# Optimization experiments

Measured on AMD Instinct MI355X. Metric: run time of the kernel, lower is better.

The kernel has to match this reference:

```python
import math
import jax, jax.numpy as jnp
import numpy as np

B, S, D, H, DK = 2, 2048, 1024, 16, 64
NUM_BUCKETS, MAX_DISTANCE = 32, 128


def _relative_position_bucket(rel_pos):
    # bidirectional=True (encoder): is_decoder=False
    nb = NUM_BUCKETS // 2
    rel_buckets = (rel_pos > 0).astype(jnp.int32) * nb
    rp = jnp.abs(rel_pos)
    max_exact = nb // 2
    is_small = rp < max_exact
    rp_large = max_exact + (
        jnp.log(rp.astype(jnp.float32) / max_exact)
        / math.log(MAX_DISTANCE / max_exact)
        * (nb - max_exact)
    ).astype(jnp.int32)
    rp_large = jnp.minimum(rp_large, nb - 1)
    return rel_buckets + jnp.where(is_small, rp, rp_large)


def compute_bias(rel_bias, q_len, k_len):
    ctx = jnp.arange(q_len, dtype=jnp.int32)[:, None]
    mem = jnp.arange(k_len, dtype=jnp.int32)[None, :]
    buckets = _relative_position_bucket(mem - ctx)          # [q,k]
    vals = rel_bias[buckets]                                 # [q,k,H]
    return jnp.transpose(vals, (2, 0, 1))[None]              # [1,H,q,k]


def setup_inputs() -> dict:
    key = jax.random.key(0)
    ks = jax.random.split(key, 6)
    scale = 0.02
    return {
        "hidden_states": jax.random.normal(ks[0], (B, S, D), jnp.float32),
        "Wq": jax.random.normal(ks[1], (D, H * DK), jnp.float32) * scale,
        "Wk": jax.random.normal(ks[2], (D, H * DK), jnp.float32) * scale,
        "Wv": jax.random.normal(ks[3], (D, H * DK), jnp.float32) * scale,
        "Wo": jax.random.normal(ks[4], (H * DK, D), jnp.float32) * scale,
        "rel_bias": jax.random.normal(ks[5], (NUM_BUCKETS, H), jnp.float32) * scale,
    }


def reference(hidden_states, Wq, Wk, Wv, Wo, rel_bias):
    b, s, _ = hidden_states.shape

    def shape(x):  # [b,s,H*DK] -> [b,H,s,DK]
        return x.reshape(b, s, H, DK).transpose(0, 2, 1, 3)

    q = shape(hidden_states @ Wq)
    k = shape(hidden_states @ Wk)
    v = shape(hidden_states @ Wv)

    # T5: no 1/sqrt(d_k) scaling
    scores = jnp.einsum("bhqd,bhkd->bhqk", q, k)
    position_bias = compute_bias(rel_bias, s, s)             # [1,H,s,s]
    scores = scores + position_bias
    attn = jax.nn.softmax(scores.astype(jnp.float32), axis=-1).astype(scores.dtype)
    out = jnp.einsum("bhqk,bhkd->bhqd", attn, v)
    out = out.transpose(0, 2, 1, 3).reshape(b, s, H * DK)
    return out @ Wo
```

## Files before the change

kernel.cpp:

```cpp
#include <hip/hip_runtime.h>

#define HH 16
#define DKK 64
#define SS 2048
#define BB 2
#define DD 1024

typedef __attribute__((ext_vector_type(4))) float f32x4;
typedef __attribute__((ext_vector_type(16))) float f32x16;
typedef __attribute__((ext_vector_type(8))) short bf16x8;
typedef __attribute__((ext_vector_type(4))) short s16x4;
typedef __attribute__((ext_vector_type(4))) int i32x4;

#define WAITCNT_VM0 0xF70

__device__ __forceinline__ short bf16b(float f) {
    union { float f; unsigned u; } x; x.f = f;
    unsigned r = (x.u + 0x7fffu + ((x.u >> 16) & 1u)) >> 16;
    return (short)r;
}

__device__ __forceinline__ f32x4 mfma16(bf16x8 a, bf16x8 b, f32x4 c) {
    return __builtin_amdgcn_mfma_f32_16x16x32_bf16(a, b, c, 0, 0, 0);
}

__device__ __forceinline__ f32x16 mfma32(bf16x8 a, bf16x8 b, f32x16 c) {
    return __builtin_amdgcn_mfma_f32_32x32x16_bf16(a, b, c, 0, 0, 0);
}

__device__ __forceinline__ void lds16(const short* g, short* l) {
    __builtin_amdgcn_global_load_lds(
        (const __attribute__((address_space(1))) void*)g,
        (__attribute__((address_space(3))) void*)l, 16, 0, 0);
}

__device__ __forceinline__ int cvtpk(float lo, float hi) {
    int r;
    asm("v_cvt_pk_bf16_f32 %0, %1, %2" : "=v"(r) : "v"(lo), "v"(hi));
    return r;
}

__device__ __forceinline__ void swap32(int& a, int& b) {
    asm("v_permlane32_swap_b32 %0, %1" : "+v"(a), "+v"(b));
}

__global__ __launch_bounds__(256) void prep(
    const float* __restrict__ hs,
    const float* __restrict__ W0, const float* __restrict__ W1,
    const float* __restrict__ W2, const float* __restrict__ W3,
    const float* __restrict__ rb,
    short* __restrict__ hsb,
    short* __restrict__ T0, short* __restrict__ T1,
    short* __restrict__ T2, short* __restrict__ T3,
    float* __restrict__ tab) {
    __shared__ short tile[32][33];
    int blk = blockIdx.x, tid = threadIdx.x;
    if (blk < 4096) {
        int i = (blk * 256 + tid) * 4;
        f32x4 v = *(const f32x4*)(hs + i);
        s16x4 o;
        o.x = bf16b(v.x); o.y = bf16b(v.y); o.z = bf16b(v.z); o.w = bf16b(v.w);
        *(s16x4*)(hsb + i) = o;
    } else if (blk < 8192) {
        int t = blk - 4096;
        int z = t >> 10, r = t & 1023;
        int bx = r & 31, by = r >> 5;
        const float* W; short* T;
        switch (z) {
            case 0: W = W0; T = T0; break;
            case 1: W = W1; T = T1; break;
            case 2: W = W2; T = T2; break;
            default: W = W3; T = T3; break;
        }
        int n0 = bx * 32, k0 = by * 32;
        int tx = tid & 31, ty = (tid >> 5) * 4;
#pragma unroll
        for (int i = 0; i < 4; i++)
            tile[ty + i][tx] = bf16b(W[(k0 + ty + i) * DD + n0 + tx]);
        __syncthreads();
#pragma unroll
        for (int i = 0; i < 4; i++)
            T[(n0 + ty + i) * DD + k0 + tx] = tile[tx][ty + i];
    } else {
        int idx = (blk - 8192) * 256 + tid;
        if (idx < HH * 4095) {
            int h = idx / 4095, d = idx % 4095;
            int rel = d - 2047;
            int bucket = (rel > 0) ? 16 : 0;
            unsigned rr = (rel < 0) ? (unsigned)(-rel) : (unsigned)rel;
            int add;
            if (rr < 8) add = (int)rr;
            else {
                int e = 31 - __clz(rr);
                unsigned long long r2 = (unsigned long long)rr * (unsigned long long)rr;
                int f = 2 * e + ((r2 >= (2ull << (2 * e))) ? 1 : 0);
                add = 8 + (f - 6);
                if (add > 15) add = 15;
            }
            bucket += add;
            tab[h * 4095 + d] = rb[bucket * HH + h] * 1.44269504f;
        }
    }
}

__global__ __launch_bounds__(256) void gemm_qkv(
    const short* __restrict__ A, const short* __restrict__ Wt,
    short* __restrict__ Cq, short* __restrict__ Ck, short* __restrict__ Cvt) {
    const int K = 1024;
    __shared__ short As[128 * 32];
    __shared__ short Bs[128 * 32];
    int tid = threadIdx.x;
    int wave = tid >> 6, lane = tid & 63;
    int quad = lane >> 4, l16 = lane & 15;
    int m0 = blockIdx.y * 128, n0 = blockIdx.x * 128;

    int wm = (wave & 1) * 64, wn = (wave >> 1) * 64;
    int r0 = tid >> 2, c0 = (tid & 3) * 8;

    f32x4 acc[4][4];
#pragma unroll
    for (int i = 0; i < 4; i++)
#pragma unroll
        for (int j = 0; j < 4; j++) acc[i][j] = (f32x4){0.f, 0.f, 0.f, 0.f};

    for (int k0 = 0; k0 < K; k0 += 32) {
        __syncthreads();
        lds16(A + (size_t)(m0 + r0) * K + k0 + c0, As + wave * 512);
        lds16(A + (size_t)(m0 + 64 + r0) * K + k0 + c0, As + 2048 + wave * 512);
        lds16(Wt + (size_t)(n0 + r0) * K + k0 + c0, Bs + wave * 512);
        lds16(Wt + (size_t)(n0 + 64 + r0) * K + k0 + c0, Bs + 2048 + wave * 512);
        __syncthreads();
        bf16x8 af[4], bfr[4];
#pragma unroll
        for (int t = 0; t < 4; t++) {
            af[t] = *(const bf16x8*)(As + (wm + t * 16 + l16) * 32 + quad * 8);
            bfr[t] = *(const bf16x8*)(Bs + (wn + t * 16 + l16) * 32 + quad * 8);
        }
#pragma unroll
        for (int mt = 0; mt < 4; mt++)
#pragma unroll
            for (int nt = 0; nt < 4; nt++)
                acc[mt][nt] = mfma16(af[mt], bfr[nt], acc[mt][nt]);
    }

#pragma unroll
    for (int mt = 0; mt < 4; mt++) {
#pragma unroll
        for (int nt = 0; nt < 4; nt++) {
#pragma unroll
            for (int r = 0; r < 4; r++) {
                int gm = m0 + wm + mt * 16 + quad * 4 + r;
                int gn = n0 + wn + nt * 16 + l16;
                int b = gm >> 11, s = gm & 2047;
                int which = gn >> 10;
                int h = (gn >> 6) & 15, dk = gn & 63;
                short bv = bf16b(acc[mt][nt][r]);
                if (which == 0)
                    Cq[(((size_t)(b * HH + h)) * SS + s) * DKK + dk] = bv;
                else if (which == 1)
                    Ck[(((size_t)(b * HH + h)) * SS + s) * DKK + dk] = bv;
                else
                    Cvt[(((size_t)(b * HH + h)) * DKK + dk) * SS + s] = bv;
            }
        }
    }
}

__global__ __launch_bounds__(256) void gemm_out(
    const short* __restrict__ A, const short* __restrict__ Wt,
    float* __restrict__ Cout) {
    const int K = 1024, N = 1024;
    __shared__ short As[64 * 32];
    __shared__ short Bs[128 * 32];
    int tid = threadIdx.x;
    int wave = tid >> 6, lane = tid & 63;
    int quad = lane >> 4, l16 = lane & 15;
    int m0 = blockIdx.y * 64, n0 = blockIdx.x * 128;

    int wm = (wave & 1) * 32, wn = (wave >> 1) * 64;
    int r0 = tid >> 2, c0 = (tid & 3) * 8;

    f32x4 acc[2][4];
#pragma unroll
    for (int i = 0; i < 2; i++)
#pragma unroll
        for (int j = 0; j < 4; j++) acc[i][j] = (f32x4){0.f, 0.f, 0.f, 0.f};

    for (int k0 = 0; k0 < K; k0 += 32) {
        __syncthreads();
        lds16(A + (size_t)(m0 + r0) * K + k0 + c0, As + wave * 512);
        lds16(Wt + (size_t)(n0 + r0) * K + k0 + c0, Bs + wave * 512);
        lds16(Wt + (size_t)(n0 + 64 + r0) * K + k0 + c0, Bs + 2048 + wave * 512);
        __syncthreads();
        bf16x8 af[2], bfr[4];
#pragma unroll
        for (int t = 0; t < 2; t++)
            af[t] = *(const bf16x8*)(As + (wm + t * 16 + l16) * 32 + quad * 8);
#pragma unroll
        for (int t = 0; t < 4; t++)
            bfr[t] = *(const bf16x8*)(Bs + (wn + t * 16 + l16) * 32 + quad * 8);
#pragma unroll
        for (int mt = 0; mt < 2; mt++)
#pragma unroll
            for (int nt = 0; nt < 4; nt++)
                acc[mt][nt] = mfma16(af[mt], bfr[nt], acc[mt][nt]);
    }

#pragma unroll
    for (int mt = 0; mt < 2; mt++)
#pragma unroll
        for (int nt = 0; nt < 4; nt++)
#pragma unroll
            for (int r = 0; r < 4; r++) {
                int gm = m0 + wm + mt * 16 + quad * 4 + r;
                int gn = n0 + wn + nt * 16 + l16;
                Cout[(size_t)gm * N + gn] = acc[mt][nt][r];
            }
}

__global__ __launch_bounds__(512, 4) void attn(
    const short* __restrict__ Q, const short* __restrict__ Kmat,
    const short* __restrict__ Vt, const float* __restrict__ btab,
    short* __restrict__ O) {
    __shared__ short Ks[2][2][64 * 64];
    __shared__ short Vs[2][2][64 * 64];

    int tid = threadIdx.x;
    int wave = tid >> 6, lane = tid & 63;
    int w4 = wave & 3, half = wave >> 2;
    int el = lane & 31, hi = lane >> 5;
    int ex7 = el & 7;
    int bh = blockIdx.x;
    int h = bh & 15, b = bh >> 4;
    int q0b = blockIdx.y * 128;
    int q0w = q0b + w4 * 32;
    int ko = half * 1024;

    const short* Qb = Q + (size_t)bh * SS * DKK;
    const short* Kb = Kmat + (size_t)bh * SS * DKK;
    const short* Vb = Vt + (size_t)bh * DKK * SS;
    const float* bt = btab + h * 4095;

    float blo = bt[2047 - 128];
    float bhi = bt[2047 + 128];

    int tid2 = tid & 255;
    int kro = tid2 >> 3;
    int gk = (tid2 & 7) ^ (kro & 7);
    const short* Kg0 = Kb + (size_t)(ko + kro) * DKK + gk * 8;
    const short* Kg1 = Kb + (size_t)(ko + kro + 32) * DKK + gk * 8;
    const short* Vg0 = Vb + (size_t)kro * SS + ko + gk * 8;
    const short* Vg1 = Vb + (size_t)(kro + 32) * SS + ko + gk * 8;

    bf16x8 qB[4];
#pragma unroll
    for (int c = 0; c < 4; c++)
        qB[c] = *(const bf16x8*)(Qb + (size_t)(q0w + el) * DKK + c * 16 + hi * 8);

    f32x16 o0, o1;
#pragma unroll
    for (int i = 0; i < 16; i++) { o0[i] = 0.f; o1[i] = 0.f; }
    float ls0 = 0.f, ls1 = 0.f, ls2 = 0.f, ls3 = 0.f;

    int bq = 2047 - q0w - el;

    lds16(Kg0, &Ks[half][0][w4 * 512]);
    lds16(Kg1, &Ks[half][0][2048 + w4 * 512]);
    lds16(Vg0, &Vs[half][0][w4 * 512]);
    lds16(Vg1, &Vs[half][0][2048 + w4 * 512]);

    int cur = 0;
    for (int kc2 = 0; kc2 < 1024; kc2 += 64) {
        __syncthreads();
        int kn2 = (kc2 + 64) & 1023;
        int nxt = cur ^ 1;
        lds16(Kg0 + (size_t)kn2 * DKK, &Ks[half][nxt][w4 * 512]);
        lds16(Kg1 + (size_t)kn2 * DKK, &Ks[half][nxt][2048 + w4 * 512]);
        lds16(Vg0 + kn2, &Vs[half][nxt][w4 * 512]);
        lds16(Vg1 + kn2, &Vs[half][nxt][2048 + w4 * 512]);

        const short* Ksc = &Ks[half][cur][0];
        const short* Vsc = &Vs[half][cur][0];

        bf16x8 vf[4][2];
#pragma unroll
        for (int c4 = 0; c4 < 4; c4++)
#pragma unroll
            for (int m = 0; m < 2; m++)
                vf[c4][m] = *(const bf16x8*)(
                    Vsc + (m * 32 + el) * 64 + (((2 * c4 + hi) ^ ex7) * 8));

#pragma unroll
        for (int st = 0; st < 2; st++) {
            f32x16 acc;
#pragma unroll
            for (int i = 0; i < 16; i++) acc[i] = 0.f;
            __builtin_amdgcn_s_setprio(1);
#pragma unroll
            for (int c = 0; c < 4; c++) {
                bf16x8 kA = *(const bf16x8*)(
                    Ksc + (st * 32 + el) * 64 + (((2 * c + hi) ^ ex7) * 8));
                acc = mfma32(kA, qB[c], acc);
            }
            __builtin_amdgcn_s_setprio(0);

            int ks = ko + kc2 + st * 32;
            float br[16];
            if (ks > q0w - 159 && ks < q0w + 159) {
#pragma unroll
                for (int r = 0; r < 16; r++)
                    br[r] = bt[bq + ks + ((r & 3) + 8 * (r >> 2) + 4 * hi)];
            } else {
                float bc = (ks <= q0w - 159) ? blo : bhi;
#pragma unroll
                for (int r = 0; r < 16; r++) br[r] = bc;
            }

            float p[16];
#pragma unroll
            for (int r = 0; r < 16; r++)
                p[r] = __builtin_amdgcn_exp2f(
                    fmaf(acc[r], 1.44269504f, br[r]));
#pragma unroll
            for (int r = 0; r < 16; r += 4) {
                ls0 += p[r]; ls1 += p[r + 1]; ls2 += p[r + 2]; ls3 += p[r + 3];
            }

            int A1 = cvtpk(p[0], p[1]),   A2 = cvtpk(p[2], p[3]);
            int B1 = cvtpk(p[4], p[5]),   B2 = cvtpk(p[6], p[7]);
            int C1 = cvtpk(p[8], p[9]),   C2 = cvtpk(p[10], p[11]);
            int D1 = cvtpk(p[12], p[13]), D2 = cvtpk(p[14], p[15]);
            swap32(A1, B1); swap32(A2, B2);
            swap32(C1, D1); swap32(C2, D2);
            bf16x8 pf0 = __builtin_bit_cast(bf16x8, (i32x4){A1, A2, B1, B2});
            bf16x8 pf1 = __builtin_bit_cast(bf16x8, (i32x4){C1, C2, D1, D2});

            __builtin_amdgcn_s_setprio(1);
            o0 = mfma32(pf0, vf[st * 2 + 0][0], o0);
            o1 = mfma32(pf0, vf[st * 2 + 0][1], o1);
            o0 = mfma32(pf1, vf[st * 2 + 1][0], o0);
            o1 = mfma32(pf1, vf[st * 2 + 1][1], o1);
            __builtin_amdgcn_s_setprio(0);
        }
        cur ^= 1;
    }
    __builtin_amdgcn_s_waitcnt(WAITCNT_VM0);

    float lsum = (ls0 + ls1) + (ls2 + ls3);
    float toth = lsum + __shfl_xor(lsum, 32);

    __syncthreads();

    float* Ob = (float*)&Ks[0][0][0];
    float* Ls = (float*)&Vs[0][0][0];
    int ex5 = lane & 31;
    int obase = (w4 * 64 + lane) * 32;

    if (half == 1) {
        if (hi == 0) Ls[w4 * 32 + el] = toth;
#pragma unroll
        for (int j = 0; j < 16; j++) {
            Ob[obase + (j ^ ex5)] = o0[j];
            Ob[obase + ((16 + j) ^ ex5)] = o1[j];
        }
    }
    __syncthreads();
    if (half == 0) {
        float tot = toth + Ls[w4 * 32 + el];
        if (hi == 0) Ls[128 + w4 * 32 + el] = 1.f / tot;
        __asm__ __volatile__("" ::: "memory");
#pragma unroll
        for (int r = 0; r < 16; r++) {
            int qm = (r & 3) + 8 * (r >> 2) + 4 * hi;
            float iv = Ls[128 + w4 * 32 + qm];
            float a0 = o0[r] + Ob[obase + (r ^ ex5)];
            float a1 = o1[r] + Ob[obase + ((16 + r) ^ ex5)];
            size_t base =
                ((size_t)(b * SS + q0w + qm)) * (HH * DKK) + h * DKK;
            O[base + el] = bf16b(a0 * iv);
            O[base + 32 + el] = bf16b(a1 * iv);
        }
    }
}

extern "C" void kernel_launch(void* const* d_in, const int* in_sizes, int n_in,
                              void* d_out, int out_size, void* d_ws, size_t ws_size,
                              hipStream_t stream) {
    const float* hs = (const float*)d_in[0];
    const float* Wq = (const float*)d_in[1];
    const float* Wk = (const float*)d_in[2];
    const float* Wv = (const float*)d_in[3];
    const float* Wo = (const float*)d_in[4];
    const float* rb = (const float*)d_in[5];
    float* out = (float*)d_out;

    char* ws = (char*)d_ws;
    size_t off = 0;
    auto alloc = [&](size_t bytes) -> void* {
        void* p = (void*)(ws + off);
        off += (bytes + 255) & ~(size_t)255;
        return p;
    };
    const size_t M = (size_t)BB * SS;
    short* hsb = (short*)alloc(M * DD * 2);
    short* WqT = (short*)alloc((size_t)DD * DD * 2);
    short* WkT = (short*)alloc((size_t)DD * DD * 2);
    short* WvT = (short*)alloc((size_t)DD * DD * 2);
    short* WoT = (short*)alloc((size_t)DD * DD * 2);
    short* Qb  = (short*)alloc(M * DD * 2);
    short* Kb  = (short*)alloc(M * DD * 2);
    short* VTb = (short*)alloc(M * DD * 2);
    short* Ab  = (short*)alloc(M * DD * 2);
    float* btab = (float*)alloc((size_t)HH * 4095 * 4);

    prep<<<8448, 256, 0, stream>>>(hs, Wq, Wk, Wv, Wo, rb,
                                   hsb, WqT, WkT, WvT, WoT, btab);
    gemm_qkv<<<dim3(24, 32), 256, 0, stream>>>(hsb, WqT, Qb, Kb, VTb);
    attn<<<dim3(32, 16), 512, 0, stream>>>(Qb, Kb, VTb, btab, Ab);
    gemm_out<<<dim3(8, 64), 256, 0, stream>>>(Ab, WoT, out);
}
```

Measured before the change: 213.5 us.

## Shrink attention blocks to 256 threads and drop LDS double buffering

The attention kernel now uses 256-thread blocks, each covering 64 queries instead of 128 and still split into two key halves, launched over twice as many blocks. The double-buffered K/V prefetch is replaced by a single buffer that is loaded, synchronised, consumed and synchronised again on every iteration. This cuts LDS use per block, which lets more blocks fit per CU and may improve occupancy. In exchange, global-to-LDS loads no longer overlap with compute, each K/V tile is loaded by half as many queries, and every iteration now has two barriers.

```diff
diff --git a/kernel.cpp b/kernel.cpp
--- a/kernel.cpp
+++ b/kernel.cpp
@@ -218,22 +218,23 @@
             }
 }
 
-__global__ __launch_bounds__(512, 4) void attn(
+__global__ __launch_bounds__(256, 4) void attn(
     const short* __restrict__ Q, const short* __restrict__ Kmat,
     const short* __restrict__ Vt, const float* __restrict__ btab,
     short* __restrict__ O) {
-    __shared__ short Ks[2][2][64 * 64];
-    __shared__ short Vs[2][2][64 * 64];
+    __shared__ short Ks[2][64 * 64];
+    __shared__ short Vs[2][64 * 64];
+    __shared__ float Ls[256];
 
     int tid = threadIdx.x;
     int wave = tid >> 6, lane = tid & 63;
-    int w4 = wave & 3, half = wave >> 2;
+    int qw = wave & 1, half = wave >> 1;
     int el = lane & 31, hi = lane >> 5;
     int ex7 = el & 7;
     int bh = blockIdx.x;
     int h = bh & 15, b = bh >> 4;
-    int q0b = blockIdx.y * 128;
-    int q0w = q0b + w4 * 32;
+    int q0b = blockIdx.y * 64;
+    int q0w = q0b + qw * 32;
     int ko = half * 1024;
 
     const short* Qb = Q + (size_t)bh * SS * DKK;
@@ -244,13 +245,12 @@
     float blo = bt[2047 - 128];
     float bhi = bt[2047 + 128];
 
-    int tid2 = tid & 255;
-    int kro = tid2 >> 3;
-    int gk = (tid2 & 7) ^ (kro & 7);
-    const short* Kg0 = Kb + (size_t)(ko + kro) * DKK + gk * 8;
-    const short* Kg1 = Kb + (size_t)(ko + kro + 32) * DKK + gk * 8;
-    const short* Vg0 = Vb + (size_t)kro * SS + ko + gk * 8;
-    const short* Vg1 = Vb + (size_t)(kro + 32) * SS + ko + gk * 8;
+    int tid_h = tid & 127;
+    int wh = tid_h >> 6;
+    int kro = tid_h >> 3;
+    int gk = (tid_h & 7) ^ (kro & 7);
+    const short* Kg = Kb + (size_t)(ko + kro) * DKK + gk * 8;
+    const short* Vg = Vb + (size_t)kro * SS + ko + gk * 8;
 
     bf16x8 qB[4];
 #pragma unroll
@@ -264,23 +264,18 @@
 
     int bq = 2047 - q0w - el;
 
-    lds16(Kg0, &Ks[half][0][w4 * 512]);
-    lds16(Kg1, &Ks[half][0][2048 + w4 * 512]);
-    lds16(Vg0, &Vs[half][0][w4 * 512]);
-    lds16(Vg1, &Vs[half][0][2048 + w4 * 512]);
-
-    int cur = 0;
     for (int kc2 = 0; kc2 < 1024; kc2 += 64) {
-        __syncthreads();
-        int kn2 = (kc2 + 64) & 1023;
-        int nxt = cur ^ 1;
-        lds16(Kg0 + (size_t)kn2 * DKK, &Ks[half][nxt][w4 * 512]);
-        lds16(Kg1 + (size_t)kn2 * DKK, &Ks[half][nxt][2048 + w4 * 512]);
-        lds16(Vg0 + kn2, &Vs[half][nxt][w4 * 512]);
-        lds16(Vg1 + kn2, &Vs[half][nxt][2048 + w4 * 512]);
-
-        const short* Ksc = &Ks[half][cur][0];
-        const short* Vsc = &Vs[half][cur][0];
+#pragma unroll
+        for (int j = 0; j < 4; j++) {
+            lds16(Kg + (size_t)(kc2 + j * 16) * DKK,
+                  &Ks[half][j * 1024 + wh * 512]);
+            lds16(Vg + kc2 + (size_t)(j * 16) * SS,
+                  &Vs[half][j * 1024 + wh * 512]);
+        }
+        __syncthreads();
+
+        const short* Ksc = &Ks[half][0];
+        const short* Vsc = &Vs[half][0];
 
         bf16x8 vf[4][2];
 #pragma unroll
@@ -342,39 +337,34 @@
             o1 = mfma32(pf1, vf[st * 2 + 1][1], o1);
             __builtin_amdgcn_s_setprio(0);
         }
-        cur ^= 1;
-    }
-    __builtin_amdgcn_s_waitcnt(WAITCNT_VM0);
+        __syncthreads();
+    }
 
     float lsum = (ls0 + ls1) + (ls2 + ls3);
     float toth = lsum + __shfl_xor(lsum, 32);
 
-    __syncthreads();
-
-    float* Ob = (float*)&Ks[0][0][0];
-    float* Ls = (float*)&Vs[0][0][0];
-    int ex5 = lane & 31;
-    int obase = (w4 * 64 + lane) * 32;
+    float* Ob = (float*)&Ks[0][0];
+    int obase = (qw * 64 + lane) * 32;
 
     if (half == 1) {
-        if (hi == 0) Ls[w4 * 32 + el] = toth;
+        if (hi == 0) Ls[qw * 32 + el] = toth;
 #pragma unroll
         for (int j = 0; j < 16; j++) {
-            Ob[obase + (j ^ ex5)] = o0[j];
-            Ob[obase + ((16 + j) ^ ex5)] = o1[j];
+            Ob[obase + (j ^ el)] = o0[j];
+            Ob[obase + ((16 + j) ^ el)] = o1[j];
         }
     }
     __syncthreads();
     if (half == 0) {
-        float tot = toth + Ls[w4 * 32 + el];
-        if (hi == 0) Ls[128 + w4 * 32 + el] = 1.f / tot;
+        float tot = toth + Ls[qw * 32 + el];
+        if (hi == 0) Ls[128 + qw * 32 + el] = 1.f / tot;
         __asm__ __volatile__("" ::: "memory");
 #pragma unroll
         for (int r = 0; r < 16; r++) {
             int qm = (r & 3) + 8 * (r >> 2) + 4 * hi;
-            float iv = Ls[128 + w4 * 32 + qm];
-            float a0 = o0[r] + Ob[obase + (r ^ ex5)];
-            float a1 = o1[r] + Ob[obase + ((16 + r) ^ ex5)];
+            float iv = Ls[128 + qw * 32 + qm];
+            float a0 = o0[r] + Ob[obase + (r ^ el)];
+            float a1 = o1[r] + Ob[obase + ((16 + r) ^ el)];
             size_t base =
                 ((size_t)(b * SS + q0w + qm)) * (HH * DKK) + h * DKK;
             O[base + el] = bf16b(a0 * iv);
@@ -416,6 +406,6 @@
     prep<<<8448, 256, 0, stream>>>(hs, Wq, Wk, Wv, Wo, rb,
                                    hsb, WqT, WkT, WvT, WoT, btab);
     gemm_qkv<<<dim3(24, 32), 256, 0, stream>>>(hsb, WqT, Qb, Kb, VTb);
-    attn<<<dim3(32, 16), 512, 0, stream>>>(Qb, Kb, VTb, btab, Ab);
+    attn<<<dim3(32, 32), 256, 0, stream>>>(Qb, Kb, VTb, btab, Ab);
     gemm_out<<<dim3(8, 64), 256, 0, stream>>>(Ab, WoT, out);
 }
```

Measured after the change: 226.0 us. 5.9% more time.
